# Optimization experiments

Hardware: AMD Instinct MI355X
Metric: run time of the kernel (lower is better)

The kernel has to match this reference:

```python
import jax, jax.numpy as jnp
import numpy as np

N = 100000
E = 1600000
D_IN = 128
D_H = 128
D_OUT = 128
LN_EPS = 1e-5
NORM_EPS = 1e-12


def _sage_conv(x, src, dst, Wl, bl, Wr):
    # PyG SAGEConv(mean): out = lin_l(mean_{j in N(i)} x_j) + lin_r(x_i)
    msgs = x[src]                                             # [E, d] gather
    summed = jax.ops.segment_sum(msgs, dst, num_segments=N)   # [N, d]
    cnt = jax.ops.segment_sum(jnp.ones((src.shape[0],), x.dtype), dst, num_segments=N)
    mean = summed / jnp.maximum(cnt, 1.0)[:, None]
    return mean @ Wl + bl + x @ Wr


def _layer_norm(x, g, b):
    mu = jnp.mean(x, axis=-1, keepdims=True)
    var = jnp.mean(jnp.square(x - mu), axis=-1, keepdims=True)
    return (x - mu) * jax.lax.rsqrt(var + LN_EPS) * g + b


def setup_inputs() -> dict:
    key = jax.random.key(0)
    ks = jax.random.split(key, 20)
    x = jax.random.normal(ks[0], (N, D_IN), dtype=jnp.float32)
    edge_index = jax.random.randint(ks[1], (2, E), 0, N, dtype=jnp.int64)
    dims = [(D_IN, D_H), (D_H, D_H), (D_H, D_OUT)]
    inp = {"x": x, "edge_index": edge_index}
    for i, (di, do) in enumerate(dims):
        s = 1.0 / np.sqrt(di)
        inp[f"Wl{i}"] = jax.random.normal(ks[2 + 5 * i], (di, do), dtype=jnp.float32) * s
        inp[f"bl{i}"] = jnp.zeros((do,), dtype=jnp.float32)
        inp[f"Wr{i}"] = jax.random.normal(ks[3 + 5 * i], (di, do), dtype=jnp.float32) * s
        inp[f"g{i}"] = jnp.ones((do,), dtype=jnp.float32)
        inp[f"b{i}"] = jnp.zeros((do,), dtype=jnp.float32)
    return inp


def reference(x, edge_index, Wl0, bl0, Wr0, g0, b0, Wl1, bl1, Wr1, g1, b1, Wl2, bl2, Wr2, g2, b2):
    src, dst = edge_index[0], edge_index[1]
    params = [(Wl0, bl0, Wr0, g0, b0), (Wl1, bl1, Wr1, g1, b1), (Wl2, bl2, Wr2, g2, b2)]
    h = x
    for i, (Wl, bl, Wr, g, b) in enumerate(params):
        h = _sage_conv(h, src, dst, Wl, bl, Wr)
        h = _layer_norm(h, g, b)
        if i < len(params) - 1:
            h = jax.nn.elu(h)
            # dropout is identity in eval mode
    # F.normalize(p=2, dim=-1)
    nrm = jnp.sqrt(jnp.sum(jnp.square(h), axis=-1, keepdims=True))
    return h / jnp.maximum(nrm, NORM_EPS)
```

## Files before the change

kernel.cpp:

```cpp
#include <hip/hip_runtime.h>
#include <hip/hip_bf16.h>
#include <math.h>

#define N_NODES 100000
#define N_EDGES 1600000
#define D 128
#define NB 391
#define BSTRIDE 6000

#define OFF_SSRC 0
#define OFF_OFFS 6400000
#define OFF_CURS 6800016
#define OFF_BSUM 7200016
#define OFF_M    7204112
#define OFF_XHI  58404112
#define OFF_XLO  84004112

typedef __attribute__((ext_vector_type(8))) short short8;
typedef __attribute__((ext_vector_type(4))) float floatx4;

__device__ __forceinline__ unsigned short f2bf(float f) {
    unsigned int u = __float_as_uint(f);
    u += 0x7fffu + ((u >> 16) & 1u);
    return (unsigned short)(u >> 16);
}
__device__ __forceinline__ float bf2f(unsigned short h) {
    return __uint_as_float(((unsigned int)h) << 16);
}

__global__ __launch_bounds__(256) void part_kernel(const int* __restrict__ src,
                                                   const int* __restrict__ dst,
                                                   int* __restrict__ gcur,
                                                   uint2* __restrict__ staging) {
    __shared__ int hist[NB];
    __shared__ int base[NB];
    int t = threadIdx.x;
    int e0 = blockIdx.x * 4096;
    for (int i = t; i < NB; i += 256) hist[i] = 0;
    __syncthreads();
    int d[16];
#pragma unroll
    for (int i = 0; i < 16; ++i) {
        int e = e0 + i * 256 + t;
        d[i] = (e < N_EDGES) ? dst[e] : -1;
        if (d[i] >= 0) atomicAdd(&hist[d[i] >> 8], 1);
    }
    __syncthreads();
    for (int i = t; i < NB; i += 256) {
        int h = hist[i];
        base[i] = h ? atomicAdd(&gcur[i], h) : 0;
    }
    __syncthreads();
    for (int i = t; i < NB; i += 256) hist[i] = 0;
    __syncthreads();
#pragma unroll
    for (int i = 0; i < 16; ++i) {
        if (d[i] >= 0) {
            int e = e0 + i * 256 + t;
            int b = d[i] >> 8;
            int slot = atomicAdd(&hist[b], 1);
            staging[b * BSTRIDE + base[b] + slot] =
                make_uint2((unsigned)src[e], (unsigned)(d[i] & 255));
        }
    }
}

__global__ void bscan_kernel(const int* __restrict__ gcur, int* __restrict__ bbase,
                             int* __restrict__ offs) {
    __shared__ int sh[512];
    int t = threadIdx.x;
    int v = (t < NB) ? gcur[t] : 0;
    sh[t] = v;
    __syncthreads();
    for (int off = 1; off < 512; off <<= 1) {
        int y = (t >= off) ? sh[t - off] : 0;
        __syncthreads();
        sh[t] += y;
        __syncthreads();
    }
    if (t < NB) bbase[t] = sh[t] - v;
    if (t == 0) offs[N_NODES] = N_EDGES;
}

__global__ __launch_bounds__(256) void bsort_kernel(const uint2* __restrict__ staging,
                                                    const int* __restrict__ gcur,
                                                    const int* __restrict__ bbase,
                                                    int* __restrict__ offs,
                                                    int* __restrict__ s_src) {
    __shared__ int cnt[256];
    __shared__ int scn[256];
    __shared__ int ssrc[BSTRIDE];
    int b = blockIdx.x;
    int t = threadIdx.x;
    int n = gcur[b];
    int base_out = bbase[b];
    cnt[t] = 0;
    __syncthreads();
    for (int e = t; e < n; e += 256) {
        uint2 v = staging[b * BSTRIDE + e];
        atomicAdd(&cnt[v.y], 1);
    }
    __syncthreads();
    int v = cnt[t];
    scn[t] = v;
    __syncthreads();
    for (int off = 1; off < 256; off <<= 1) {
        int y = (t >= off) ? scn[t - off] : 0;
        __syncthreads();
        scn[t] += y;
        __syncthreads();
    }
    int ex = scn[t] - v;
    int node = b * 256 + t;
    if (node < N_NODES) offs[node] = base_out + ex;
    cnt[t] = ex;
    __syncthreads();
    for (int e = t; e < n; e += 256) {
        uint2 w = staging[b * BSTRIDE + e];
        int slot = atomicAdd(&cnt[w.y], 1);
        ssrc[slot] = (int)w.x;
    }
    __syncthreads();
    for (int e = t; e < n; e += 256) s_src[base_out + e] = ssrc[e];
}

__global__ void pack_kernel(const float* __restrict__ Wl0, const float* __restrict__ Wr0,
                            const float* __restrict__ Wl1, const float* __restrict__ Wr1,
                            const float* __restrict__ Wl2, const float* __restrict__ Wr2,
                            unsigned short* __restrict__ pack) {
    int tid = blockIdx.x * blockDim.x + threadIdx.x;
    int l = tid >> 15;
    int r = tid & 32767;
    int k = r >> 7;
    int n = r & 127;
    const float* Wl = (l == 0) ? Wl0 : (l == 1) ? Wl1 : Wl2;
    const float* Wr = (l == 0) ? Wr0 : (l == 1) ? Wr1 : Wr2;
    float v = (k < 128) ? Wl[k * 128 + n] : Wr[(k - 128) * 128 + n];
    unsigned short hi = f2bf(v);
    unsigned short lo = f2bf(v - bf2f(hi));
    int ct = n >> 4, ks = k >> 5, lane = ((k >> 3) & 3) * 16 + (n & 15), j = k & 7;
    int idx = ((ct * 8 + ks) * 64 + lane) * 8 + j;
    pack[l * 65536 + idx] = hi;
    pack[l * 65536 + 32768 + idx] = lo;
}

__global__ __launch_bounds__(256) void cvt_kernel(const float* __restrict__ x,
                                                  unsigned int* __restrict__ Xhi,
                                                  unsigned int* __restrict__ Xlo) {
    int i = blockIdx.x * 256 + threadIdx.x;
    float2 v = ((const float2*)x)[i];
    unsigned short h0 = f2bf(v.x), h1 = f2bf(v.y);
    unsigned short l0 = f2bf(v.x - bf2f(h0)), l1 = f2bf(v.y - bf2f(h1));
    Xhi[i] = (unsigned int)h0 | ((unsigned int)h1 << 16);
    Xlo[i] = (unsigned int)l0 | ((unsigned int)l1 << 16);
}

__global__ __launch_bounds__(256) void agg_kernel(const unsigned int* __restrict__ Xhi,
                                                  const int* __restrict__ s_src,
                                                  const int* __restrict__ offs,
                                                  float* __restrict__ mean) {
    int wid = threadIdx.x >> 6, lane = threadIdx.x & 63;
    int node = blockIdx.x * 4 + wid;
    int beg = offs[node], end = offs[node + 1];
    float a0 = 0.f, a1 = 0.f, b0 = 0.f, b1 = 0.f;
    int e = beg;
    for (; e + 3 < end; e += 4) {
        int s0 = s_src[e], s1 = s_src[e + 1], s2 = s_src[e + 2], s3 = s_src[e + 3];
        unsigned int u0 = Xhi[s0 * 64 + lane];
        unsigned int u1 = Xhi[s1 * 64 + lane];
        unsigned int u2 = Xhi[s2 * 64 + lane];
        unsigned int u3 = Xhi[s3 * 64 + lane];
        a0 += bf2f((unsigned short)u0) + bf2f((unsigned short)u1);
        a1 += bf2f((unsigned short)(u0 >> 16)) + bf2f((unsigned short)(u1 >> 16));
        b0 += bf2f((unsigned short)u2) + bf2f((unsigned short)u3);
        b1 += bf2f((unsigned short)(u2 >> 16)) + bf2f((unsigned short)(u3 >> 16));
    }
    for (; e < end; ++e) {
        unsigned int u = Xhi[s_src[e] * 64 + lane];
        a0 += bf2f((unsigned short)u);
        a1 += bf2f((unsigned short)(u >> 16));
    }
    float inv = 1.0f / fmaxf((float)(end - beg), 1.0f);
    ((float2*)mean)[node * 64 + lane] = make_float2((a0 + b0) * inv, (a1 + b1) * inv);
}

__global__ __launch_bounds__(256) void mmln_kernel(unsigned short* Xh,
                                                   unsigned short* Xl,
                                                   const float* __restrict__ mean,
                                                   const unsigned short* __restrict__ packh,
                                                   const unsigned short* __restrict__ packl,
                                                   const float* __restrict__ bl,
                                                   const float* __restrict__ g,
                                                   const float* __restrict__ b,
                                                   float* __restrict__ outf, int last) {
    int t = threadIdx.x;
    int lane = t & 63;
    int wid = t >> 6;
    int colb = lane & 15;
    int quad = lane >> 4;
    int kq = quad * 8;
    int tilebase = blockIdx.x * 128 + wid * 32;

    int rowA[2];
    rowA[0] = min(tilebase + colb, N_NODES - 1);
    rowA[1] = min(tilebase + 16 + colb, N_NODES - 1);

    floatx4 acc[2][8];
#pragma unroll
    for (int rt = 0; rt < 2; ++rt)
#pragma unroll
        for (int ct = 0; ct < 8; ++ct) acc[rt][ct] = (floatx4){0.f, 0.f, 0.f, 0.f};

#pragma unroll
    for (int ks = 0; ks < 4; ++ks) {
        int kof = ks * 32 + kq;
        short8 ah[2], al[2];
#pragma unroll
        for (int rt = 0; rt < 2; ++rt) {
            const float* p = mean + (long)rowA[rt] * D + kof;
            float4 v0 = *(const float4*)p;
            float4 v1 = *(const float4*)(p + 4);
            float v[8] = {v0.x, v0.y, v0.z, v0.w, v1.x, v1.y, v1.z, v1.w};
#pragma unroll
            for (int j = 0; j < 8; ++j) {
                unsigned short hi = f2bf(v[j]);
                ah[rt][j] = (short)hi;
                al[rt][j] = (short)f2bf(v[j] - bf2f(hi));
            }
        }
#pragma unroll
        for (int ct = 0; ct < 8; ++ct) {
            int fo = ((ct * 8 + ks) << 9) + (lane << 3);
            short8 bh = *(const short8*)(packh + fo);
            short8 bo = *(const short8*)(packl + fo);
#pragma unroll
            for (int rt = 0; rt < 2; ++rt) {
                acc[rt][ct] = __builtin_amdgcn_mfma_f32_16x16x32_bf16(ah[rt], bh, acc[rt][ct], 0, 0, 0);
                acc[rt][ct] = __builtin_amdgcn_mfma_f32_16x16x32_bf16(al[rt], bh, acc[rt][ct], 0, 0, 0);
                acc[rt][ct] = __builtin_amdgcn_mfma_f32_16x16x32_bf16(ah[rt], bo, acc[rt][ct], 0, 0, 0);
            }
        }
    }
#pragma unroll
    for (int ks = 4; ks < 8; ++ks) {
        int kof = (ks - 4) * 32 + kq;
        short8 ah[2], al[2];
#pragma unroll
        for (int rt = 0; rt < 2; ++rt) {
            long o = (long)rowA[rt] * D + kof;
            ah[rt] = *(const short8*)(Xh + o);
            al[rt] = *(const short8*)(Xl + o);
        }
#pragma unroll
        for (int ct = 0; ct < 8; ++ct) {
            int fo = ((ct * 8 + ks) << 9) + (lane << 3);
            short8 bh = *(const short8*)(packh + fo);
            short8 bo = *(const short8*)(packl + fo);
#pragma unroll
            for (int rt = 0; rt < 2; ++rt) {
                acc[rt][ct] = __builtin_amdgcn_mfma_f32_16x16x32_bf16(ah[rt], bh, acc[rt][ct], 0, 0, 0);
                acc[rt][ct] = __builtin_amdgcn_mfma_f32_16x16x32_bf16(al[rt], bh, acc[rt][ct], 0, 0, 0);
                acc[rt][ct] = __builtin_amdgcn_mfma_f32_16x16x32_bf16(ah[rt], bo, acc[rt][ct], 0, 0, 0);
            }
        }
    }

    float bb[8], gg[8], b2[8];
#pragma unroll
    for (int ct = 0; ct < 8; ++ct) {
        bb[ct] = bl[ct * 16 + colb];
        gg[ct] = g[ct * 16 + colb];
        b2[ct] = b[ct * 16 + colb];
    }

#pragma unroll
    for (int rt = 0; rt < 2; ++rt) {
#pragma unroll
        for (int ct = 0; ct < 8; ++ct)
#pragma unroll
            for (int e = 0; e < 4; ++e) acc[rt][ct][e] += bb[ct];
        float mu[4], rstd[4];
#pragma unroll
        for (int e = 0; e < 4; ++e) {
            float s = 0.f;
#pragma unroll
            for (int ct = 0; ct < 8; ++ct) s += acc[rt][ct][e];
            s += __shfl_xor(s, 1); s += __shfl_xor(s, 2);
            s += __shfl_xor(s, 4); s += __shfl_xor(s, 8);
            mu[e] = s * (1.0f / 128.0f);
        }
#pragma unroll
        for (int e = 0; e < 4; ++e) {
            float q = 0.f;
#pragma unroll
            for (int ct = 0; ct < 8; ++ct) {
                float d = acc[rt][ct][e] - mu[e];
                q += d * d;
            }
            q += __shfl_xor(q, 1); q += __shfl_xor(q, 2);
            q += __shfl_xor(q, 4); q += __shfl_xor(q, 8);
            rstd[e] = rsqrtf(q * (1.0f / 128.0f) + 1e-5f);
        }
#pragma unroll
        for (int ct = 0; ct < 8; ++ct)
#pragma unroll
            for (int e = 0; e < 4; ++e) {
                float y = (acc[rt][ct][e] - mu[e]) * rstd[e] * gg[ct] + b2[ct];
                if (!last) y = (y > 0.f) ? y : expm1f(y);
                acc[rt][ct][e] = y;
            }
        if (last) {
#pragma unroll
            for (int e = 0; e < 4; ++e) {
                float ss = 0.f;
#pragma unroll
                for (int ct = 0; ct < 8; ++ct) {
                    float y = acc[rt][ct][e];
                    ss += y * y;
                }
                ss += __shfl_xor(ss, 1); ss += __shfl_xor(ss, 2);
                ss += __shfl_xor(ss, 4); ss += __shfl_xor(ss, 8);
                float inv = 1.0f / fmaxf(sqrtf(ss), 1e-12f);
#pragma unroll
                for (int ct = 0; ct < 8; ++ct) acc[rt][ct][e] *= inv;
            }
#pragma unroll
            for (int e = 0; e < 4; ++e) {
                int row = tilebase + rt * 16 + quad * 4 + e;
                if (row < N_NODES) {
#pragma unroll
                    for (int ct = 0; ct < 8; ++ct)
                        outf[(long)row * D + ct * 16 + colb] = acc[rt][ct][e];
                }
            }
        } else {
#pragma unroll
            for (int e = 0; e < 4; ++e) {
                int row = tilebase + rt * 16 + quad * 4 + e;
                if (row < N_NODES) {
#pragma unroll
                    for (int ct = 0; ct < 8; ++ct) {
                        float y = acc[rt][ct][e];
                        unsigned short hh = f2bf(y);
                        unsigned short ll = f2bf(y - bf2f(hh));
                        long o = (long)row * D + ct * 16 + colb;
                        Xh[o] = hh;
                        Xl[o] = ll;
                    }
                }
            }
        }
    }
}

extern "C" void kernel_launch(void* const* d_in, const int* in_sizes, int n_in,
                              void* d_out, int out_size, void* d_ws, size_t ws_size,
                              hipStream_t stream) {
    const float* x = (const float*)d_in[0];
    const int* edges = (const int*)d_in[1];
    const int* src = edges;
    const int* dst = edges + N_EDGES;
    const float* Wl[3] = {(const float*)d_in[2], (const float*)d_in[7],  (const float*)d_in[12]};
    const float* bl[3] = {(const float*)d_in[3], (const float*)d_in[8],  (const float*)d_in[13]};
    const float* Wr[3] = {(const float*)d_in[4], (const float*)d_in[9],  (const float*)d_in[14]};
    const float* g[3]  = {(const float*)d_in[5], (const float*)d_in[10], (const float*)d_in[15]};
    const float* b[3]  = {(const float*)d_in[6], (const float*)d_in[11], (const float*)d_in[16]};

    char* ws = (char*)d_ws;
    int* s_src = (int*)(ws + OFF_SSRC);
    int* offs  = (int*)(ws + OFF_OFFS);
    unsigned short* wpack = (unsigned short*)(ws + OFF_CURS);
    int* gcur  = (int*)(ws + OFF_BSUM);
    int* bbase = (int*)(ws + OFF_BSUM + 2048);
    float* M = (float*)(ws + OFF_M);
    uint2* staging = (uint2*)(ws + OFF_M);
    unsigned short* Xhi = (unsigned short*)(ws + OFF_XHI);
    unsigned short* Xlo = (unsigned short*)(ws + OFF_XLO);
    float* out = (float*)d_out;

    hipMemsetAsync(gcur, 0, NB * sizeof(int), stream);
    part_kernel<<<(N_EDGES + 4095) / 4096, 256, 0, stream>>>(src, dst, gcur, staging);
    bscan_kernel<<<1, 512, 0, stream>>>(gcur, bbase, offs);
    bsort_kernel<<<NB, 256, 0, stream>>>(staging, gcur, bbase, offs, s_src);
    pack_kernel<<<(3 * 32768) / 256, 256, 0, stream>>>(Wl[0], Wr[0], Wl[1], Wr[1], Wl[2], Wr[2], wpack);
    cvt_kernel<<<(N_NODES * 64) / 256, 256, 0, stream>>>(x, (unsigned int*)Xhi, (unsigned int*)Xlo);

    const int MMB = (N_NODES + 127) / 128;
    unsigned short* ph[3] = {wpack, wpack + 65536, wpack + 131072};

    agg_kernel<<<N_NODES / 4, 256, 0, stream>>>((const unsigned int*)Xhi, s_src, offs, M);
    mmln_kernel<<<MMB, 256, 0, stream>>>(Xhi, Xlo, M, ph[0], ph[0] + 32768, bl[0], g[0], b[0], nullptr, 0);
    agg_kernel<<<N_NODES / 4, 256, 0, stream>>>((const unsigned int*)Xhi, s_src, offs, M);
    mmln_kernel<<<MMB, 256, 0, stream>>>(Xhi, Xlo, M, ph[1], ph[1] + 32768, bl[1], g[1], b[1], nullptr, 0);
    agg_kernel<<<N_NODES / 4, 256, 0, stream>>>((const unsigned int*)Xhi, s_src, offs, M);
    mmln_kernel<<<MMB, 256, 0, stream>>>(Xhi, Xlo, M, ph[2], ph[2] + 32768, bl[2], g[2], b[2], out, 1);
}
```

Measured before the change: 647.7 us.

## Fuse neighbor mean aggregation into the matmul+LayerNorm kernel via LDS

Each wave now gathers and averages the neighbor features for its 16 rows, keeps the means in shared memory, and feeds them straight into the MFMA matmul and LayerNorm epilogue. This removes the separate aggregation kernel and the round trip of a full fp32 mean matrix through global memory each layer. Ping-pong hi/lo feature buffers replace in-place updates, and the MFMA row tile shrinks from 32 to 16 rows. In exchange, each wave processes its nodes one after another, which lowers gather memory-level parallelism, cuts the number of blocks, and doubles weight fetches per row.

After: 709.2 us. 1.09x slower.

```diff
diff --git a/kernel.cpp b/kernel.cpp
--- a/kernel.cpp
+++ b/kernel.cpp
@@ -10,11 +10,13 @@
 
 #define OFF_SSRC 0
 #define OFF_OFFS 6400000
-#define OFF_CURS 6800016
-#define OFF_BSUM 7200016
-#define OFF_M    7204112
-#define OFF_XHI  58404112
-#define OFF_XLO  84004112
+#define OFF_PACK 6800016
+#define OFF_GC   7193232
+#define OFF_BB   7195296
+#define OFF_AH   7200000
+#define OFF_AL   32800000
+#define OFF_BH   58400000
+#define OFF_BL   84000000
 
 typedef __attribute__((ext_vector_type(8))) short short8;
 typedef __attribute__((ext_vector_type(4))) float floatx4;
@@ -155,113 +157,97 @@
     Xlo[i] = (unsigned int)l0 | ((unsigned int)l1 << 16);
 }
 
-__global__ __launch_bounds__(256) void agg_kernel(const unsigned int* __restrict__ Xhi,
-                                                  const int* __restrict__ s_src,
-                                                  const int* __restrict__ offs,
-                                                  float* __restrict__ mean) {
-    int wid = threadIdx.x >> 6, lane = threadIdx.x & 63;
-    int node = blockIdx.x * 4 + wid;
-    int beg = offs[node], end = offs[node + 1];
-    float a0 = 0.f, a1 = 0.f, b0 = 0.f, b1 = 0.f;
-    int e = beg;
-    for (; e + 3 < end; e += 4) {
-        int s0 = s_src[e], s1 = s_src[e + 1], s2 = s_src[e + 2], s3 = s_src[e + 3];
-        unsigned int u0 = Xhi[s0 * 64 + lane];
-        unsigned int u1 = Xhi[s1 * 64 + lane];
-        unsigned int u2 = Xhi[s2 * 64 + lane];
-        unsigned int u3 = Xhi[s3 * 64 + lane];
-        a0 += bf2f((unsigned short)u0) + bf2f((unsigned short)u1);
-        a1 += bf2f((unsigned short)(u0 >> 16)) + bf2f((unsigned short)(u1 >> 16));
-        b0 += bf2f((unsigned short)u2) + bf2f((unsigned short)u3);
-        b1 += bf2f((unsigned short)(u2 >> 16)) + bf2f((unsigned short)(u3 >> 16));
-    }
-    for (; e < end; ++e) {
-        unsigned int u = Xhi[s_src[e] * 64 + lane];
-        a0 += bf2f((unsigned short)u);
-        a1 += bf2f((unsigned short)(u >> 16));
-    }
-    float inv = 1.0f / fmaxf((float)(end - beg), 1.0f);
-    ((float2*)mean)[node * 64 + lane] = make_float2((a0 + b0) * inv, (a1 + b1) * inv);
-}
-
-__global__ __launch_bounds__(256) void mmln_kernel(unsigned short* Xh,
-                                                   unsigned short* Xl,
-                                                   const float* __restrict__ mean,
-                                                   const unsigned short* __restrict__ packh,
-                                                   const unsigned short* __restrict__ packl,
-                                                   const float* __restrict__ bl,
-                                                   const float* __restrict__ g,
-                                                   const float* __restrict__ b,
-                                                   float* __restrict__ outf, int last) {
+__global__ __launch_bounds__(256) void fused_kernel(const unsigned short* __restrict__ Xh,
+                                                    const unsigned short* __restrict__ Xl,
+                                                    const int* __restrict__ s_src,
+                                                    const int* __restrict__ offs,
+                                                    const unsigned short* __restrict__ packh,
+                                                    const unsigned short* __restrict__ packl,
+                                                    const float* __restrict__ bl,
+                                                    const float* __restrict__ g,
+                                                    const float* __restrict__ b,
+                                                    unsigned short* __restrict__ Yh,
+                                                    unsigned short* __restrict__ Yl,
+                                                    float* __restrict__ outf, int last) {
+    __shared__ float mlds[4][16][132];
     int t = threadIdx.x;
     int lane = t & 63;
     int wid = t >> 6;
+    int tilebase = blockIdx.x * 64 + wid * 16;
+    const unsigned int* Xh32 = (const unsigned int*)Xh;
+
+    for (int r = 0; r < 16; ++r) {
+        int node = tilebase + r;
+        if (node >= N_NODES) break;
+        int beg = offs[node], end = offs[node + 1];
+        float a0 = 0.f, a1 = 0.f, b0 = 0.f, b1 = 0.f;
+        int e = beg;
+        for (; e + 3 < end; e += 4) {
+            int s0 = s_src[e], s1 = s_src[e + 1], s2 = s_src[e + 2], s3 = s_src[e + 3];
+            unsigned int u0 = Xh32[s0 * 64 + lane];
+            unsigned int u1 = Xh32[s1 * 64 + lane];
+            unsigned int u2 = Xh32[s2 * 64 + lane];
+            unsigned int u3 = Xh32[s3 * 64 + lane];
+            a0 += bf2f((unsigned short)u0) + bf2f((unsigned short)u1);
+            a1 += bf2f((unsigned short)(u0 >> 16)) + bf2f((unsigned short)(u1 >> 16));
+            b0 += bf2f((unsigned short)u2) + bf2f((unsigned short)u3);
+            b1 += bf2f((unsigned short)(u2 >> 16)) + bf2f((unsigned short)(u3 >> 16));
+        }
+        for (; e < end; ++e) {
+            unsigned int u = Xh32[s_src[e] * 64 + lane];
+            a0 += bf2f((unsigned short)u);
+            a1 += bf2f((unsigned short)(u >> 16));
+        }
+        float inv = 1.0f / fmaxf((float)(end - beg), 1.0f);
+        mlds[wid][r][lane * 2] = (a0 + b0) * inv;
+        mlds[wid][r][lane * 2 + 1] = (a1 + b1) * inv;
+    }
+
     int colb = lane & 15;
     int quad = lane >> 4;
     int kq = quad * 8;
-    int tilebase = blockIdx.x * 128 + wid * 32;
-
-    int rowA[2];
-    rowA[0] = min(tilebase + colb, N_NODES - 1);
-    rowA[1] = min(tilebase + 16 + colb, N_NODES - 1);
-
-    floatx4 acc[2][8];
-#pragma unroll
-    for (int rt = 0; rt < 2; ++rt)
-#pragma unroll
-        for (int ct = 0; ct < 8; ++ct) acc[rt][ct] = (floatx4){0.f, 0.f, 0.f, 0.f};
+    int rowA = min(tilebase + colb, N_NODES - 1);
+
+    floatx4 acc[8];
+#pragma unroll
+    for (int ct = 0; ct < 8; ++ct) acc[ct] = (floatx4){0.f, 0.f, 0.f, 0.f};
 
 #pragma unroll
     for (int ks = 0; ks < 4; ++ks) {
-        int kof = ks * 32 + kq;
-        short8 ah[2], al[2];
-#pragma unroll
-        for (int rt = 0; rt < 2; ++rt) {
-            const float* p = mean + (long)rowA[rt] * D + kof;
-            float4 v0 = *(const float4*)p;
-            float4 v1 = *(const float4*)(p + 4);
-            float v[8] = {v0.x, v0.y, v0.z, v0.w, v1.x, v1.y, v1.z, v1.w};
-#pragma unroll
-            for (int j = 0; j < 8; ++j) {
-                unsigned short hi = f2bf(v[j]);
-                ah[rt][j] = (short)hi;
-                al[rt][j] = (short)f2bf(v[j] - bf2f(hi));
-            }
+        const float* p = &mlds[wid][colb][ks * 32 + kq];
+        float4 v0 = *(const float4*)p;
+        float4 v1 = *(const float4*)(p + 4);
+        float v[8] = {v0.x, v0.y, v0.z, v0.w, v1.x, v1.y, v1.z, v1.w};
+        short8 ah, al;
+#pragma unroll
+        for (int j = 0; j < 8; ++j) {
+            unsigned short hi = f2bf(v[j]);
+            ah[j] = (short)hi;
+            al[j] = (short)f2bf(v[j] - bf2f(hi));
         }
 #pragma unroll
         for (int ct = 0; ct < 8; ++ct) {
             int fo = ((ct * 8 + ks) << 9) + (lane << 3);
             short8 bh = *(const short8*)(packh + fo);
             short8 bo = *(const short8*)(packl + fo);
-#pragma unroll
-            for (int rt = 0; rt < 2; ++rt) {
-                acc[rt][ct] = __builtin_amdgcn_mfma_f32_16x16x32_bf16(ah[rt], bh, acc[rt][ct], 0, 0, 0);
-                acc[rt][ct] = __builtin_amdgcn_mfma_f32_16x16x32_bf16(al[rt], bh, acc[rt][ct], 0, 0, 0);
-                acc[rt][ct] = __builtin_amdgcn_mfma_f32_16x16x32_bf16(ah[rt], bo, acc[rt][ct], 0, 0, 0);
-            }
+            acc[ct] = __builtin_amdgcn_mfma_f32_16x16x32_bf16(ah, bh, acc[ct], 0, 0, 0);
+            acc[ct] = __builtin_amdgcn_mfma_f32_16x16x32_bf16(al, bh, acc[ct], 0, 0, 0);
+            acc[ct] = __builtin_amdgcn_mfma_f32_16x16x32_bf16(ah, bo, acc[ct], 0, 0, 0);
         }
     }
 #pragma unroll
     for (int ks = 4; ks < 8; ++ks) {
-        int kof = (ks - 4) * 32 + kq;
-        short8 ah[2], al[2];
-#pragma unroll
-        for (int rt = 0; rt < 2; ++rt) {
-            long o = (long)rowA[rt] * D + kof;
-            ah[rt] = *(const short8*)(Xh + o);
-            al[rt] = *(const short8*)(Xl + o);
-        }
+        long o = (long)rowA * D + (ks - 4) * 32 + kq;
+        short8 ah = *(const short8*)(Xh + o);
+        short8 al = *(const short8*)(Xl + o);
 #pragma unroll
         for (int ct = 0; ct < 8; ++ct) {
             int fo = ((ct * 8 + ks) << 9) + (lane << 3);
             short8 bh = *(const short8*)(packh + fo);
             short8 bo = *(const short8*)(packl + fo);
-#pragma unroll
-            for (int rt = 0; rt < 2; ++rt) {
-                acc[rt][ct] = __builtin_amdgcn_mfma_f32_16x16x32_bf16(ah[rt], bh, acc[rt][ct], 0, 0, 0);
-                acc[rt][ct] = __builtin_amdgcn_mfma_f32_16x16x32_bf16(al[rt], bh, acc[rt][ct], 0, 0, 0);
-                acc[rt][ct] = __builtin_amdgcn_mfma_f32_16x16x32_bf16(ah[rt], bo, acc[rt][ct], 0, 0, 0);
-            }
+            acc[ct] = __builtin_amdgcn_mfma_f32_16x16x32_bf16(ah, bh, acc[ct], 0, 0, 0);
+            acc[ct] = __builtin_amdgcn_mfma_f32_16x16x32_bf16(al, bh, acc[ct], 0, 0, 0);
+            acc[ct] = __builtin_amdgcn_mfma_f32_16x16x32_bf16(ah, bo, acc[ct], 0, 0, 0);
         }
     }
 
@@ -272,81 +258,78 @@
         gg[ct] = g[ct * 16 + colb];
         b2[ct] = b[ct * 16 + colb];
     }
-
-#pragma unroll
-    for (int rt = 0; rt < 2; ++rt) {
-#pragma unroll
-        for (int ct = 0; ct < 8; ++ct)
-#pragma unroll
-            for (int e = 0; e < 4; ++e) acc[rt][ct][e] += bb[ct];
-        float mu[4], rstd[4];
+#pragma unroll
+    for (int ct = 0; ct < 8; ++ct)
+#pragma unroll
+        for (int e = 0; e < 4; ++e) acc[ct][e] += bb[ct];
+
+    float mu[4], rstd[4];
+#pragma unroll
+    for (int e = 0; e < 4; ++e) {
+        float s = 0.f;
+#pragma unroll
+        for (int ct = 0; ct < 8; ++ct) s += acc[ct][e];
+        s += __shfl_xor(s, 1); s += __shfl_xor(s, 2);
+        s += __shfl_xor(s, 4); s += __shfl_xor(s, 8);
+        mu[e] = s * (1.0f / 128.0f);
+    }
+#pragma unroll
+    for (int e = 0; e < 4; ++e) {
+        float q = 0.f;
+#pragma unroll
+        for (int ct = 0; ct < 8; ++ct) {
+            float d = acc[ct][e] - mu[e];
+            q += d * d;
+        }
+        q += __shfl_xor(q, 1); q += __shfl_xor(q, 2);
+        q += __shfl_xor(q, 4); q += __shfl_xor(q, 8);
+        rstd[e] = rsqrtf(q * (1.0f / 128.0f) + 1e-5f);
+    }
+#pragma unroll
+    for (int ct = 0; ct < 8; ++ct)
 #pragma unroll
         for (int e = 0; e < 4; ++e) {
-            float s = 0.f;
-#pragma unroll
-            for (int ct = 0; ct < 8; ++ct) s += acc[rt][ct][e];
-            s += __shfl_xor(s, 1); s += __shfl_xor(s, 2);
-            s += __shfl_xor(s, 4); s += __shfl_xor(s, 8);
-            mu[e] = s * (1.0f / 128.0f);
-        }
+            float y = (acc[ct][e] - mu[e]) * rstd[e] * gg[ct] + b2[ct];
+            if (!last) y = (y > 0.f) ? y : expm1f(y);
+            acc[ct][e] = y;
+        }
+    if (last) {
 #pragma unroll
         for (int e = 0; e < 4; ++e) {
-            float q = 0.f;
+            float ss = 0.f;
 #pragma unroll
             for (int ct = 0; ct < 8; ++ct) {
-                float d = acc[rt][ct][e] - mu[e];
-                q += d * d;
+                float y = acc[ct][e];
+                ss += y * y;
             }
-            q += __shfl_xor(q, 1); q += __shfl_xor(q, 2);
-            q += __shfl_xor(q, 4); q += __shfl_xor(q, 8);
-            rstd[e] = rsqrtf(q * (1.0f / 128.0f) + 1e-5f);
-        }
-#pragma unroll
-        for (int ct = 0; ct < 8; ++ct)
-#pragma unroll
-            for (int e = 0; e < 4; ++e) {
-                float y = (acc[rt][ct][e] - mu[e]) * rstd[e] * gg[ct] + b2[ct];
-                if (!last) y = (y > 0.f) ? y : expm1f(y);
-                acc[rt][ct][e] = y;
+            ss += __shfl_xor(ss, 1); ss += __shfl_xor(ss, 2);
+            ss += __shfl_xor(ss, 4); ss += __shfl_xor(ss, 8);
+            float inv = 1.0f / fmaxf(sqrtf(ss), 1e-12f);
+#pragma unroll
+            for (int ct = 0; ct < 8; ++ct) acc[ct][e] *= inv;
+        }
+#pragma unroll
+        for (int e = 0; e < 4; ++e) {
+            int row = tilebase + quad * 4 + e;
+            if (row < N_NODES) {
+#pragma unroll
+                for (int ct = 0; ct < 8; ++ct)
+                    outf[(long)row * D + ct * 16 + colb] = acc[ct][e];
             }
-        if (last) {
-#pragma unroll
-            for (int e = 0; e < 4; ++e) {
-                float ss = 0.f;
+        }
+    } else {
+#pragma unroll
+        for (int e = 0; e < 4; ++e) {
+            int row = tilebase + quad * 4 + e;
+            if (row < N_NODES) {
 #pragma unroll
                 for (int ct = 0; ct < 8; ++ct) {
-                    float y = acc[rt][ct][e];
-                    ss += y * y;
-                }
-                ss += __shfl_xor(ss, 1); ss += __shfl_xor(ss, 2);
-                ss += __shfl_xor(ss, 4); ss += __shfl_xor(ss, 8);
-                float inv = 1.0f / fmaxf(sqrtf(ss), 1e-12f);
-#pragma unroll
-                for (int ct = 0; ct < 8; ++ct) acc[rt][ct][e] *= inv;
-            }
-#pragma unroll
-            for (int e = 0; e < 4; ++e) {
-                int row = tilebase + rt * 16 + quad * 4 + e;
-                if (row < N_NODES) {
-#pragma unroll
-                    for (int ct = 0; ct < 8; ++ct)
-                        outf[(long)row * D + ct * 16 + colb] = acc[rt][ct][e];
-                }
-            }
-        } else {
-#pragma unroll
-            for (int e = 0; e < 4; ++e) {
-                int row = tilebase + rt * 16 + quad * 4 + e;
-                if (row < N_NODES) {
-#pragma unroll
-                    for (int ct = 0; ct < 8; ++ct) {
-                        float y = acc[rt][ct][e];
-                        unsigned short hh = f2bf(y);
-                        unsigned short ll = f2bf(y - bf2f(hh));
-                        long o = (long)row * D + ct * 16 + colb;
-                        Xh[o] = hh;
-                        Xl[o] = ll;
-                    }
+                    float y = acc[ct][e];
+                    unsigned short hh = f2bf(y);
+                    unsigned short ll = f2bf(y - bf2f(hh));
+                    long o = (long)row * D + ct * 16 + colb;
+                    Yh[o] = hh;
+                    Yl[o] = ll;
                 }
             }
         }
@@ -369,13 +352,14 @@
     char* ws = (char*)d_ws;
     int* s_src = (int*)(ws + OFF_SSRC);
     int* offs  = (int*)(ws + OFF_OFFS);
-    unsigned short* wpack = (unsigned short*)(ws + OFF_CURS);
-    int* gcur  = (int*)(ws + OFF_BSUM);
-    int* bbase = (int*)(ws + OFF_BSUM + 2048);
-    float* M = (float*)(ws + OFF_M);
-    uint2* staging = (uint2*)(ws + OFF_M);
-    unsigned short* Xhi = (unsigned short*)(ws + OFF_XHI);
-    unsigned short* Xlo = (unsigned short*)(ws + OFF_XLO);
+    unsigned short* wpack = (unsigned short*)(ws + OFF_PACK);
+    int* gcur  = (int*)(ws + OFF_GC);
+    int* bbase = (int*)(ws + OFF_BB);
+    unsigned short* AH = (unsigned short*)(ws + OFF_AH);
+    unsigned short* AL = (unsigned short*)(ws + OFF_AL);
+    unsigned short* BH = (unsigned short*)(ws + OFF_BH);
+    unsigned short* BL = (unsigned short*)(ws + OFF_BL);
+    uint2* staging = (uint2*)(ws + OFF_BH);
     float* out = (float*)d_out;
 
     hipMemsetAsync(gcur, 0, NB * sizeof(int), stream);
@@ -383,15 +367,15 @@
     bscan_kernel<<<1, 512, 0, stream>>>(gcur, bbase, offs);
     bsort_kernel<<<NB, 256, 0, stream>>>(staging, gcur, bbase, offs, s_src);
     pack_kernel<<<(3 * 32768) / 256, 256, 0, stream>>>(Wl[0], Wr[0], Wl[1], Wr[1], Wl[2], Wr[2], wpack);
-    cvt_kernel<<<(N_NODES * 64) / 256, 256, 0, stream>>>(x, (unsigned int*)Xhi, (unsigned int*)Xlo);
-
-    const int MMB = (N_NODES + 127) / 128;
+    cvt_kernel<<<(N_NODES * 64) / 256, 256, 0, stream>>>(x, (unsigned int*)AH, (unsigned int*)AL);
+
+    const int FB = (N_NODES + 63) / 64;
     unsigned short* ph[3] = {wpack, wpack + 65536, wpack + 131072};
 
-    agg_kernel<<<N_NODES / 4, 256, 0, stream>>>((const unsigned int*)Xhi, s_src, offs, M);
-    mmln_kernel<<<MMB, 256, 0, stream>>>(Xhi, Xlo, M, ph[0], ph[0] + 32768, bl[0], g[0], b[0], nullptr, 0);
-    agg_kernel<<<N_NODES / 4, 256, 0, stream>>>((const unsigned int*)Xhi, s_src, offs, M);
-    mmln_kernel<<<MMB, 256, 0, stream>>>(Xhi, Xlo, M, ph[1], ph[1] + 32768, bl[1], g[1], b[1], nullptr, 0);
-    agg_kernel<<<N_NODES / 4, 256, 0, stream>>>((const unsigned int*)Xhi, s_src, offs, M);
-    mmln_kernel<<<MMB, 256, 0, stream>>>(Xhi, Xlo, M, ph[2], ph[2] + 32768, bl[2], g[2], b[2], out, 1);
-}
+    fused_kernel<<<FB, 256, 0, stream>>>(AH, AL, s_src, offs, ph[0], ph[0] + 32768,
+                                         bl[0], g[0], b[0], BH, BL, nullptr, 0);
+    fused_kernel<<<FB, 256, 0, stream>>>(BH, BL, s_src, offs, ph[1], ph[1] + 32768,
+                                         bl[1], g[1], b[1], AH, AL, nullptr, 0);
+    fused_kernel<<<FB, 256, 0, stream>>>(AH, AL, s_src, offs, ph[2], ph[2] + 32768,
+                                         bl[2], g[2], b[2], nullptr, nullptr, out, 1);
+}
```
